# Optimization experiments

Measured on AMD Instinct MI355X. Metric: run time of the kernel, lower is better.

## Reference

```python
import jax, jax.numpy as jnp
import numpy as np


def maxpool2x2(x):
    # NCHW 2x2 max pool, stride 2
    return jax.lax.reduce_window(x, -jnp.inf, jax.lax.max, (1, 1, 2, 2), (1, 1, 2, 2), 'VALID')


def _xavier_uniform(k, shape):
    fan_out, fan_in = shape
    lim = np.sqrt(6.0 / (fan_in + fan_out))
    return jax.random.uniform(k, shape, jnp.float32, -lim, lim)


def setup_inputs() -> dict:
    key = jax.random.key(0)
    ks = jax.random.split(key, 5)
    C = 64
    x = jax.random.normal(ks[0], (4, C, 128, 128), jnp.float32)
    Wq = _xavier_uniform(ks[1], (C // 8, C))  # 1x1 conv == channel matmul
    Wk = _xavier_uniform(ks[2], (C // 8, C))
    Wv = _xavier_uniform(ks[3], (C // 2, C))
    Wo = _xavier_uniform(ks[4], (C, C // 2))
    gamma = jnp.full((1,), 0.1, jnp.float32)  # nonzero so attention branch contributes
    return {"x": x, "Wq": Wq, "Wk": Wk, "Wv": Wv, "Wo": Wo, "gamma": gamma}


def reference(x, Wq, Wk, Wv, Wo, gamma):
    b, c, w, h = x.shape
    # 1x1 convs as channel contractions
    q = jnp.einsum('oc,bchw->bohw', Wq, x).reshape(b, c // 8, w * h)          # [b, c/8, k]
    k_ = maxpool2x2(jnp.einsum('oc,bchw->bohw', Wk, x)).reshape(b, c // 8, -1)  # [b, c/8, f]
    v = maxpool2x2(jnp.einsum('oc,bchw->bohw', Wv, x)).reshape(b, c // 2, -1)   # [b, c/2, f]
    # softmax over full-resolution query positions k (last axis), per pooled position f
    weights = jax.nn.softmax(jnp.einsum('bcf,bck->bfk', k_, q), axis=-1)        # [b, f, k]
    out = jnp.einsum('bcf,bfk->bck', v, weights).reshape(b, c // 2, w, h)       # [b, c/2, w, h]
    out = jnp.einsum('oc,bchw->bohw', Wo, out)                                   # [b, c, w, h]
    return gamma * out + x
```

## Files before the change

### kernel.cpp

```cpp
#include <hip/hip_runtime.h>
#include <cstdint>
#include <cstddef>


#define LOG2E 1.44269504088896340736f
#define FE_A 8388608.0f
#define FE_B 1064993098.0f

typedef __attribute__((ext_vector_type(8)))  __bf16 bf8_t;
typedef __attribute__((ext_vector_type(16))) float  fx16;

__device__ __forceinline__ unsigned short f2bf(float f) {
  unsigned int u = __builtin_bit_cast(unsigned int, f);
  u += 0x7FFFu + ((u >> 16) & 1u);
  return (unsigned short)(u >> 16);
}
__device__ __forceinline__ unsigned int pk2(unsigned short lo, unsigned short hi) {
  return (unsigned int)lo | ((unsigned int)hi << 16);
}
__device__ __forceinline__ int pi16(int s) {
  int m = (s >> 2) & 3;
  return (m == 1 || m == 2) ? (s ^ 12) : s;
}
__device__ __forceinline__ unsigned fe_u(float s) {
  return (unsigned)fmaf(s, FE_A, FE_B);
}
__device__ __forceinline__ float fe_f(float s) {
  return __builtin_bit_cast(float, fe_u(s));
}
__device__ __forceinline__ unsigned fe_pk(float s0, float s1) {
  return __builtin_amdgcn_perm(fe_u(s1), fe_u(s0), 0x07060302);
}

__global__ void __launch_bounds__(512) k_qkv(const float* __restrict__ x,
                                             const float* __restrict__ Wq,
                                             const float* __restrict__ Wk,
                                             const float* __restrict__ Wv,
                                             const float* __restrict__ Wo,
                                             unsigned short* __restrict__ Qp,
                                             unsigned short* __restrict__ KpB,
                                             float* __restrict__ Vp,
                                             unsigned short* __restrict__ Wop) {
  if (blockIdx.x == 256) {
    for (int i = threadIdx.x; i < 2048; i += 512) {
      int c = i & 31;
      Wop[i] = f2bf(Wo[(i & ~31) | (c & 16) | pi16(c & 15)]);
    }
    return;
  }
  __shared__ float wst[64][48];
  __shared__ float xs[16][256];
  int t = threadIdx.x;
  for (int i = t; i < 512; i += 512) {
    wst[i & 63][i >> 6] = Wq[i];
    wst[i & 63][8 + (i >> 6)] = Wk[i];
  }
  for (int i = t; i < 2048; i += 512) wst[i & 63][16 + (i >> 6)] = Wv[i];
  int b = blockIdx.x >> 6, frow = blockIdx.x & 63;
  int wvx = t >> 6, rg = wvx & 3, h = wvx >> 2;
  int lane = t & 63, c2 = lane >> 1, cpos = lane & 1;
  int cell = h * 32 + c2, col = h * 64 + lane;
  const float* xb = x + (size_t)b * (64 * 16384) + frow * 256;
  float acc[12][2];
#pragma unroll
  for (int j = 0; j < 12; ++j) { acc[j][0] = 0.f; acc[j][1] = 0.f; }
  int cl = t >> 5, seg = t & 31;
  for (int cc = 0; cc < 4; ++cc) {
    __syncthreads();
    const float4* src =
        reinterpret_cast<const float4*>(xb + (size_t)(cc * 16 + cl) * 16384 + seg * 8);
    float4* dst = reinterpret_cast<float4*>(&xs[cl][seg * 8]);
    dst[0] = src[0]; dst[1] = src[1];
    __syncthreads();
#pragma unroll
    for (int c16 = 0; c16 < 16; ++c16) {
      int c = cc * 16 + c16;
      float xa = xs[c16][col], xo = xs[c16][128 + col];
      float4 w0 = *reinterpret_cast<const float4*>(&wst[c][12 * rg]);
      float4 w1 = *reinterpret_cast<const float4*>(&wst[c][12 * rg + 4]);
      float4 w2 = *reinterpret_cast<const float4*>(&wst[c][12 * rg + 8]);
      float wj[12] = {w0.x, w0.y, w0.z, w0.w, w1.x, w1.y, w1.z, w1.w,
                      w2.x, w2.y, w2.z, w2.w};
#pragma unroll
      for (int j = 0; j < 12; ++j) {
        acc[j][0] = fmaf(wj[j], xa, acc[j][0]);
        acc[j][1] = fmaf(wj[j], xo, acc[j][1]);
      }
    }
  }
  float pm[12];
#pragma unroll
  for (int j = 0; j < 12; ++j) {
    pm[j] = fmaxf(acc[j][0], acc[j][1]);
    pm[j] = fmaxf(pm[j], __shfl_xor(pm[j], 1));
  }
  size_t idx = (size_t)b * 4096 + frow * 64 + cell;
  uint4 z4; z4.x = z4.y = z4.z = z4.w = 0u;
  if (rg == 0) {
#pragma unroll
    for (int p = 0; p < 2; ++p) {
      int kpos = frow * 256 + p * 128 + col;
      uint4 qa;
      qa.x = pk2(f2bf(acc[0][p]), f2bf(acc[1][p]));
      qa.y = pk2(f2bf(acc[2][p]), f2bf(acc[3][p]));
      qa.z = pk2(f2bf(acc[4][p]), f2bf(acc[5][p]));
      qa.w = pk2(f2bf(acc[6][p]), f2bf(acc[7][p]));
      uint4* qdst = reinterpret_cast<uint4*>(Qp + ((size_t)b * 16384 + kpos) * 16);
      qdst[0] = qa; qdst[1] = z4;
    }
    if (cpos == 0) {
      uint2 kw;
      kw.x = pk2(f2bf(pm[8] * LOG2E), f2bf(pm[9] * LOG2E));
      kw.y = pk2(f2bf(pm[10] * LOG2E), f2bf(pm[11] * LOG2E));
      *reinterpret_cast<uint2*>(KpB + idx * 16) = kw;
    }
  } else if (rg == 1) {
    if (cpos == 0) {
      uint2 kw;
      kw.x = pk2(f2bf(pm[0] * LOG2E), f2bf(pm[1] * LOG2E));
      kw.y = pk2(f2bf(pm[2] * LOG2E), f2bf(pm[3] * LOG2E));
      *reinterpret_cast<uint2*>(KpB + idx * 16 + 4) = kw;
      *reinterpret_cast<uint4*>(KpB + idx * 16 + 8) = z4;
      float* vd = Vp + idx * 32;
      *reinterpret_cast<float4*>(vd) = make_float4(pm[4], pm[5], pm[6], pm[7]);
      *reinterpret_cast<float4*>(vd + 4) = make_float4(pm[8], pm[9], pm[10], pm[11]);
    }
  } else if (cpos == 0) {
    float* vd = Vp + idx * 32 + (rg == 2 ? 8 : 20);
#pragma unroll
    for (int j4 = 0; j4 < 3; ++j4)
      *reinterpret_cast<float4*>(vd + 4 * j4) =
          make_float4(pm[4 * j4], pm[4 * j4 + 1], pm[4 * j4 + 2], pm[4 * j4 + 3]);
  }
}

__global__ void __launch_bounds__(1024) k_lsum(const unsigned short* __restrict__ Qp,
                                               const unsigned short* __restrict__ KpB,
                                               float* __restrict__ Lpart) {
  int b = blockIdx.x >> 8, r = blockIdx.x & 255;
  int fg = r >> 1, kh = r & 1;
  int wv = threadIdx.x >> 6, lane = threadIdx.x & 63;
  int half = lane >> 5, l31 = lane & 31;
  bf8_t A = *reinterpret_cast<const bf8_t*>(
      KpB + ((size_t)(b * 4096 + fg * 32 + l31)) * 16 + half * 8);
  const unsigned short* qbase = Qp + ((size_t)b * 16384) * 16 + half * 8;
  fx16 z;
#pragma unroll
  for (int i = 0; i < 16; ++i) z[i] = 0.f;
  float l[16];
#pragma unroll
  for (int i = 0; i < 16; ++i) l[i] = 0.f;
  int t0 = kh * 256 + wv * 16;
  bf8_t B = *reinterpret_cast<const bf8_t*>(qbase + (size_t)(t0 * 32 + l31) * 16);
  for (int i = 0; i < 16; ++i) {
    int tn = t0 + ((i + 1) & 15);
    bf8_t nB = *reinterpret_cast<const bf8_t*>(qbase + (size_t)(tn * 32 + l31) * 16);
    fx16 s = __builtin_amdgcn_mfma_f32_32x32x16_bf16(A, B, z, 0, 0, 0);
#pragma unroll
    for (int r0 = 0; r0 < 16; ++r0) l[r0] += fe_f(s[r0]);
    B = nB;
  }
#pragma unroll
  for (int r0 = 0; r0 < 16; ++r0)
    for (int d = 1; d < 32; d <<= 1) l[r0] += __shfl_xor(l[r0], d);
  __shared__ float sl[16][32];
  if (l31 == 0) {
#pragma unroll
    for (int r0 = 0; r0 < 16; ++r0) {
      int row = (r0 & 3) + 8 * (r0 >> 2) + 4 * half;
      sl[wv][row] = l[r0];
    }
  }
  __syncthreads();
  if (threadIdx.x < 32) {
    float L = 0.f;
#pragma unroll
    for (int w2 = 0; w2 < 16; ++w2) L += sl[w2][threadIdx.x];
    Lpart[(size_t)kh * 16384 + b * 4096 + fg * 32 + threadIdx.x] = L;
  }
}

__global__ void __launch_bounds__(256) k_pack(const float* __restrict__ Vp,
                                              const float* __restrict__ Lpart,
                                              unsigned short* __restrict__ Vpp) {
  int b = blockIdx.x >> 4, f0 = (blockIdx.x & 15) * 256;
  __shared__ unsigned short T[32][264];
  int t = threadIdx.x;
  size_t li = (size_t)b * 4096 + f0 + t;
  float rl = 1.0f / (Lpart[li] + Lpart[16384 + li]);
  const float* vp = Vp + li * 32;
  int fl = (t & ~15) | pi16(t & 15);
  for (int c = 0; c < 32; ++c) T[c][fl] = f2bf(vp[c] * rl);
  __syncthreads();
  for (int u = t; u < 1024; u += 256) {
    int row = u >> 5, e0 = (u & 31) * 8;
    uint4 val = *reinterpret_cast<const uint4*>(&T[row][e0]);
    *reinterpret_cast<uint4*>(Vpp + ((size_t)b * 32 + row) * 4096 + f0 + e0) = val;
  }
}

__global__ void __launch_bounds__(512) k_attn(const unsigned short* __restrict__ Qp,
                                              const unsigned short* __restrict__ KpB,
                                              const unsigned short* __restrict__ Vpp,
                                              const unsigned short* __restrict__ Wop,
                                              const float* __restrict__ x,
                                              const float* __restrict__ gamma,
                                              float* __restrict__ out) {
  int b = blockIdx.x >> 8, kp = blockIdx.x & 255;
  int wv = threadIdx.x >> 6, lane = threadIdx.x & 63;
  int half = lane >> 5, l31 = lane & 31;
  int kbase = kp * 64;
  const unsigned short* qb = Qp + ((size_t)b * 16384 + kbase + l31) * 16 + half * 8;
  bf8_t Bq0 = *reinterpret_cast<const bf8_t*>(qb);
  bf8_t Bq1 = *reinterpret_cast<const bf8_t*>(qb + 32 * 16);
  fx16 z;
#pragma unroll
  for (int i = 0; i < 16; ++i) z[i] = 0.f;
  fx16 acc0 = z, acc1 = z;
  const unsigned short* kpB = KpB + ((size_t)b * 4096 + l31) * 16 + half * 8;
  const unsigned short* vpB = Vpp + ((size_t)(b * 32 + l31)) * 4096 + half * 8;
  int c0 = wv * 16;
  int f0 = c0 * 32;
  bf8_t Ak  = *reinterpret_cast<const bf8_t*>(kpB + (size_t)f0 * 16);
  bf8_t Av0 = *reinterpret_cast<const bf8_t*>(vpB + f0);
  bf8_t Av1 = *reinterpret_cast<const bf8_t*>(vpB + f0 + 16);
  for (int fc = 0; fc < 16; ++fc) {
    int f1 = (c0 + ((fc + 1) & 15)) * 32;
    bf8_t nAk  = *reinterpret_cast<const bf8_t*>(kpB + (size_t)f1 * 16);
    bf8_t nAv0 = *reinterpret_cast<const bf8_t*>(vpB + f1);
    bf8_t nAv1 = *reinterpret_cast<const bf8_t*>(vpB + f1 + 16);
    fx16 s0 = __builtin_amdgcn_mfma_f32_32x32x16_bf16(Ak, Bq0, z, 0, 0, 0);
    fx16 s1 = __builtin_amdgcn_mfma_f32_32x32x16_bf16(Ak, Bq1, z, 0, 0, 0);
    uint4 u00, u01, u10, u11;
    u00.x = fe_pk(s0[0], s0[1]);   u00.y = fe_pk(s0[2], s0[3]);
    u00.z = fe_pk(s0[4], s0[5]);   u00.w = fe_pk(s0[6], s0[7]);
    u01.x = fe_pk(s0[8], s0[9]);   u01.y = fe_pk(s0[10], s0[11]);
    u01.z = fe_pk(s0[12], s0[13]); u01.w = fe_pk(s0[14], s0[15]);
    u10.x = fe_pk(s1[0], s1[1]);   u10.y = fe_pk(s1[2], s1[3]);
    u10.z = fe_pk(s1[4], s1[5]);   u10.w = fe_pk(s1[6], s1[7]);
    u11.x = fe_pk(s1[8], s1[9]);   u11.y = fe_pk(s1[10], s1[11]);
    u11.z = fe_pk(s1[12], s1[13]); u11.w = fe_pk(s1[14], s1[15]);
    bf8_t P00 = __builtin_bit_cast(bf8_t, u00);
    bf8_t P01 = __builtin_bit_cast(bf8_t, u01);
    bf8_t P10 = __builtin_bit_cast(bf8_t, u10);
    bf8_t P11 = __builtin_bit_cast(bf8_t, u11);
    acc0 = __builtin_amdgcn_mfma_f32_32x32x16_bf16(Av0, P00, acc0, 0, 0, 0);
    acc1 = __builtin_amdgcn_mfma_f32_32x32x16_bf16(Av0, P10, acc1, 0, 0, 0);
    acc0 = __builtin_amdgcn_mfma_f32_32x32x16_bf16(Av1, P01, acc0, 0, 0, 0);
    acc1 = __builtin_amdgcn_mfma_f32_32x32x16_bf16(Av1, P11, acc1, 0, 0, 0);
    Ak = nAk; Av0 = nAv0; Av1 = nAv1;
  }
  __shared__ float sacc[4][2][4][64][4];
  if (wv >= 4) {
    int s = wv - 4;
#pragma unroll
    for (int j4 = 0; j4 < 4; ++j4) {
      *reinterpret_cast<float4*>(&sacc[s][0][j4][lane][0]) =
          make_float4(acc0[4 * j4], acc0[4 * j4 + 1], acc0[4 * j4 + 2], acc0[4 * j4 + 3]);
      *reinterpret_cast<float4*>(&sacc[s][1][j4][lane][0]) =
          make_float4(acc1[4 * j4], acc1[4 * j4 + 1], acc1[4 * j4 + 2], acc1[4 * j4 + 3]);
    }
  }
  __syncthreads();
  if (wv >= 4) return;
  int kt = wv & 1, ot = wv >> 1;
  int k = kbase + kt * 32 + l31;
  const float* xp = x + (size_t)b * 64 * 16384 + k;
  float xv[16];
#pragma unroll
  for (int r0 = 0; r0 < 16; ++r0) {
    int row = (r0 & 3) + 8 * (r0 >> 2) + 4 * half + ot * 32;
    xv[r0] = xp[(size_t)row * 16384];
  }
#pragma unroll
  for (int j4 = 0; j4 < 4; ++j4) {
    float4 p0 = *reinterpret_cast<const float4*>(&sacc[wv][0][j4][lane][0]);
    float4 p1 = *reinterpret_cast<const float4*>(&sacc[wv][1][j4][lane][0]);
    p0.x += acc0[4 * j4]; p0.y += acc0[4 * j4 + 1];
    p0.z += acc0[4 * j4 + 2]; p0.w += acc0[4 * j4 + 3];
    p1.x += acc1[4 * j4]; p1.y += acc1[4 * j4 + 1];
    p1.z += acc1[4 * j4 + 2]; p1.w += acc1[4 * j4 + 3];
    *reinterpret_cast<float4*>(&sacc[wv][0][j4][lane][0]) = p0;
    *reinterpret_cast<float4*>(&sacc[wv][1][j4][lane][0]) = p1;
  }
  __syncthreads();
  fx16 tot;
#pragma unroll
  for (int j4 = 0; j4 < 4; ++j4) {
    float4 a0 = *reinterpret_cast<const float4*>(&sacc[0][kt][j4][lane][0]);
    float4 a1 = *reinterpret_cast<const float4*>(&sacc[1][kt][j4][lane][0]);
    float4 a2 = *reinterpret_cast<const float4*>(&sacc[2][kt][j4][lane][0]);
    float4 a3 = *reinterpret_cast<const float4*>(&sacc[3][kt][j4][lane][0]);
    tot[4 * j4]     = (a0.x + a1.x) + (a2.x + a3.x);
    tot[4 * j4 + 1] = (a0.y + a1.y) + (a2.y + a3.y);
    tot[4 * j4 + 2] = (a0.z + a1.z) + (a2.z + a3.z);
    tot[4 * j4 + 3] = (a0.w + a1.w) + (a2.w + a3.w);
  }
  bf8_t Ob0, Ob1;
#pragma unroll
  for (int j = 0; j < 8; ++j) { Ob0[j] = (__bf16)tot[j]; Ob1[j] = (__bf16)tot[8 + j]; }
  const unsigned short* wb = Wop + (ot * 32 + l31) * 32 + half * 8;
  bf8_t Aw0 = *reinterpret_cast<const bf8_t*>(wb);
  bf8_t Aw1 = *reinterpret_cast<const bf8_t*>(wb + 16);
  fx16 y = __builtin_amdgcn_mfma_f32_32x32x16_bf16(Aw0, Ob0, z, 0, 0, 0);
  y = __builtin_amdgcn_mfma_f32_32x32x16_bf16(Aw1, Ob1, y, 0, 0, 0);
  float g = gamma[0];
  float* op = out + (size_t)b * 64 * 16384 + k;
#pragma unroll
  for (int r0 = 0; r0 < 16; ++r0) {
    int row = (r0 & 3) + 8 * (r0 >> 2) + 4 * half + ot * 32;
    op[(size_t)row * 16384] = fmaf(g, y[r0], xv[r0]);
  }
}

extern "C" void kernel_launch(void* const* d_in, const int* in_sizes, int n_in,
                              void* d_out, int out_size, void* d_ws, size_t ws_size,
                              hipStream_t stream) {
  const float* x     = (const float*)d_in[0];
  const float* Wq    = (const float*)d_in[1];
  const float* Wk    = (const float*)d_in[2];
  const float* Wv    = (const float*)d_in[3];
  const float* Wo    = (const float*)d_in[4];
  const float* gamma = (const float*)d_in[5];
  float* out = (float*)d_out;
  char* ws = (char*)d_ws;
  unsigned short* Qp    = (unsigned short*)(ws + 0);
  unsigned short* KpB   = (unsigned short*)(ws + 2097152);
  float*          Vp    = (float*)(ws + 2621440);
  unsigned short* Vpp   = (unsigned short*)(ws + 4718592);
  float*          Lpart = (float*)(ws + 5767168);
  unsigned short* Wop   = (unsigned short*)(ws + 5898240);

  k_qkv <<<dim3(257),  dim3(512),  0, stream>>>(x, Wq, Wk, Wv, Wo, Qp, KpB, Vp, Wop);
  k_lsum<<<dim3(1024), dim3(1024), 0, stream>>>(Qp, KpB, Lpart);
  k_pack<<<dim3(64),   dim3(256),  0, stream>>>(Vp, Lpart, Vpp);
  k_attn<<<dim3(1024), dim3(512),  0, stream>>>(Qp, KpB, Vpp, Wop, x, gamma, out);
}
```

Before: 154.0 us.

## Use split-bf16 MFMA for QKV projection and retile lsum/attn blocks

The QKV projection moves from scalar FMA to MFMA, using a hi/lo bf16 split (three MFMAs per step) to keep near-fp32 accuracy, with x staged in swizzled LDS. The log-sum kernel now has each wave handle two K tiles over 32 Q tiles, with four partial sums per row instead of two. The attention kernel drops to 256-thread blocks where each wave covers 32 f-chunks, and a final wave computes both output-channel halves, removing one LDS reduction round. The aim is to cut ALU time in the projection and reduce block-level reduction and synchronisation overhead, at the cost of more register pressure and less parallelism per block.

After: 154.4 us. About the same (+0.3%).

```diff
diff --git a/kernel.cpp b/kernel.cpp
--- a/kernel.cpp
+++ b/kernel.cpp
@@ -15,6 +15,10 @@
   u += 0x7FFFu + ((u >> 16) & 1u);
   return (unsigned short)(u >> 16);
 }
+__device__ __forceinline__ float bf2f(unsigned short h) {
+  unsigned int u = ((unsigned int)h) << 16;
+  return __builtin_bit_cast(float, u);
+}
 __device__ __forceinline__ unsigned int pk2(unsigned short lo, unsigned short hi) {
   return (unsigned int)lo | ((unsigned int)hi << 16);
 }
@@ -31,6 +35,8 @@
 __device__ __forceinline__ unsigned fe_pk(float s0, float s1) {
   return __builtin_amdgcn_perm(fe_u(s1), fe_u(s0), 0x07060302);
 }
+
+#define MFMA __builtin_amdgcn_mfma_f32_32x32x16_bf16
 
 __global__ void __launch_bounds__(512) k_qkv(const float* __restrict__ x,
                                              const float* __restrict__ Wq,
@@ -48,135 +54,168 @@
     }
     return;
   }
-  __shared__ float wst[64][48];
-  __shared__ float xs[16][256];
+  __shared__ unsigned int xs[256 * 64];
   int t = threadIdx.x;
-  for (int i = t; i < 512; i += 512) {
-    wst[i & 63][i >> 6] = Wq[i];
-    wst[i & 63][8 + (i >> 6)] = Wk[i];
-  }
-  for (int i = t; i < 2048; i += 512) wst[i & 63][16 + (i >> 6)] = Wv[i];
-  int b = blockIdx.x >> 6, frow = blockIdx.x & 63;
-  int wvx = t >> 6, rg = wvx & 3, h = wvx >> 2;
-  int lane = t & 63, c2 = lane >> 1, cpos = lane & 1;
-  int cell = h * 32 + c2, col = h * 64 + lane;
-  const float* xb = x + (size_t)b * (64 * 16384) + frow * 256;
-  float acc[12][2];
-#pragma unroll
-  for (int j = 0; j < 12; ++j) { acc[j][0] = 0.f; acc[j][1] = 0.f; }
-  int cl = t >> 5, seg = t & 31;
-  for (int cc = 0; cc < 4; ++cc) {
-    __syncthreads();
-    const float4* src =
-        reinterpret_cast<const float4*>(xb + (size_t)(cc * 16 + cl) * 16384 + seg * 8);
-    float4* dst = reinterpret_cast<float4*>(&xs[cl][seg * 8]);
-    dst[0] = src[0]; dst[1] = src[1];
-    __syncthreads();
-#pragma unroll
-    for (int c16 = 0; c16 < 16; ++c16) {
-      int c = cc * 16 + c16;
-      float xa = xs[c16][col], xo = xs[c16][128 + col];
-      float4 w0 = *reinterpret_cast<const float4*>(&wst[c][12 * rg]);
-      float4 w1 = *reinterpret_cast<const float4*>(&wst[c][12 * rg + 4]);
-      float4 w2 = *reinterpret_cast<const float4*>(&wst[c][12 * rg + 8]);
-      float wj[12] = {w0.x, w0.y, w0.z, w0.w, w1.x, w1.y, w1.z, w1.w,
-                      w2.x, w2.y, w2.z, w2.w};
-#pragma unroll
-      for (int j = 0; j < 12; ++j) {
-        acc[j][0] = fmaf(wj[j], xa, acc[j][0]);
-        acc[j][1] = fmaf(wj[j], xo, acc[j][1]);
-      }
-    }
-  }
-  float pm[12];
-#pragma unroll
-  for (int j = 0; j < 12; ++j) {
-    pm[j] = fmaxf(acc[j][0], acc[j][1]);
-    pm[j] = fmaxf(pm[j], __shfl_xor(pm[j], 1));
-  }
-  size_t idx = (size_t)b * 4096 + frow * 64 + cell;
-  uint4 z4; z4.x = z4.y = z4.z = z4.w = 0u;
-  if (rg == 0) {
-#pragma unroll
-    for (int p = 0; p < 2; ++p) {
-      int kpos = frow * 256 + p * 128 + col;
-      uint4 qa;
-      qa.x = pk2(f2bf(acc[0][p]), f2bf(acc[1][p]));
-      qa.y = pk2(f2bf(acc[2][p]), f2bf(acc[3][p]));
-      qa.z = pk2(f2bf(acc[4][p]), f2bf(acc[5][p]));
-      qa.w = pk2(f2bf(acc[6][p]), f2bf(acc[7][p]));
-      uint4* qdst = reinterpret_cast<uint4*>(Qp + ((size_t)b * 16384 + kpos) * 16);
-      qdst[0] = qa; qdst[1] = z4;
-    }
-    if (cpos == 0) {
+  int b = blockIdx.x >> 6, T = blockIdx.x & 63;
+  {
+    int pos = t & 255, cslot = t >> 8;
+    const float* xb = x + (size_t)b * (64 * 16384) + T * 256 + pos;
+    int sw = pos & 15;
+    unsigned int* row = xs + pos * 64;
+#pragma unroll
+    for (int i = 0; i < 16; ++i) {
+      int p = cslot * 16 + i;
+      float g0 = xb[(size_t)(2 * p) * 16384];
+      float g1 = xb[(size_t)(2 * p + 1) * 16384];
+      unsigned short h0 = f2bf(g0), h1 = f2bf(g1);
+      unsigned short l0 = f2bf(g0 - bf2f(h0)), l1 = f2bf(g1 - bf2f(h1));
+      int q = p >> 2, d = p & 3;
+      row[((q + sw) & 15) * 4 + d] = pk2(h0, h1);
+      row[((q + 8 + sw) & 15) * 4 + d] = pk2(l0, l1);
+    }
+  }
+  int wv = t >> 6, lane = t & 63;
+  int cg = wv & 3, Mt = wv >> 2;
+  int m = lane & 31, h = lane >> 5;
+  const float* wrow;
+  float scale = 1.0f;
+  bool zero = false;
+  if (Mt == 0) {
+    if (m < 8) wrow = Wq + m * 64;
+    else if (m < 16) { wrow = Wk + (m - 8) * 64; scale = LOG2E; }
+    else wrow = Wv + (m - 16) * 64;
+  } else {
+    if (m < 16) wrow = Wv + (m + 16) * 64;
+    else { wrow = Wq; zero = true; }
+  }
+  bf8_t Ahi[4], Alo[4];
+#pragma unroll
+  for (int kk = 0; kk < 4; ++kk) {
+    unsigned short hi8[8], lo8[8];
+#pragma unroll
+    for (int j = 0; j < 8; ++j) {
+      float w = zero ? 0.f : wrow[kk * 16 + h * 8 + j] * scale;
+      unsigned short wh = f2bf(w);
+      hi8[j] = wh;
+      lo8[j] = f2bf(w - bf2f(wh));
+    }
+    uint4 uh, ul;
+    uh.x = pk2(hi8[0], hi8[1]); uh.y = pk2(hi8[2], hi8[3]);
+    uh.z = pk2(hi8[4], hi8[5]); uh.w = pk2(hi8[6], hi8[7]);
+    ul.x = pk2(lo8[0], lo8[1]); ul.y = pk2(lo8[2], lo8[3]);
+    ul.z = pk2(lo8[4], lo8[5]); ul.w = pk2(lo8[6], lo8[7]);
+    Ahi[kk] = __builtin_bit_cast(bf8_t, uh);
+    Alo[kk] = __builtin_bit_cast(bf8_t, ul);
+  }
+  __syncthreads();
+  fx16 z;
+#pragma unroll
+  for (int i = 0; i < 16; ++i) z[i] = 0.f;
+  fx16 D0 = z, D1 = z;
+#pragma unroll
+  for (int r = 0; r < 2; ++r) {
+    fx16 acc = z;
+    int pos = cg * 32 + r * 128 + (lane & 31);
+    const unsigned int* row = xs + pos * 64;
+    int sw = pos & 15;
+#pragma unroll
+    for (int kk = 0; kk < 4; ++kk) {
+      int q = 2 * kk + h;
+      bf8_t Bh = *reinterpret_cast<const bf8_t*>(&row[((q + sw) & 15) * 4]);
+      bf8_t Bl = *reinterpret_cast<const bf8_t*>(&row[((q + 8 + sw) & 15) * 4]);
+      acc = MFMA(Ahi[kk], Bh, acc, 0, 0, 0);
+      acc = MFMA(Ahi[kk], Bl, acc, 0, 0, 0);
+      acc = MFMA(Alo[kk], Bh, acc, 0, 0, 0);
+    }
+    if (r == 0) D0 = acc; else D1 = acc;
+  }
+  uint2 z2; z2.x = z2.y = 0u;
+  if (Mt == 0) {
+#pragma unroll
+    for (int r = 0; r < 2; ++r) {
+      const fx16& D = r ? D1 : D0;
+      int gpos = T * 256 + r * 128 + cg * 32 + (lane & 31);
+      unsigned short* qd = Qp + ((size_t)b * 16384 + gpos) * 16;
+      uint2 qa;
+      qa.x = pk2(f2bf(D[0]), f2bf(D[1]));
+      qa.y = pk2(f2bf(D[2]), f2bf(D[3]));
+      *reinterpret_cast<uint2*>(qd + h * 4) = qa;
+      *reinterpret_cast<uint2*>(qd + 8 + h * 4) = z2;
+    }
+  }
+  float pm[16];
+#pragma unroll
+  for (int r0 = 0; r0 < 16; ++r0) {
+    float a = fmaxf(D0[r0], __shfl_xor(D0[r0], 1));
+    float bb = fmaxf(D1[r0], __shfl_xor(D1[r0], 1));
+    pm[r0] = fmaxf(a, bb);
+  }
+  if ((lane & 1) == 0) {
+    size_t idx = (size_t)b * 4096 + T * 64 + cg * 16 + ((lane & 31) >> 1);
+    float* vd = Vp + idx * 32;
+    if (Mt == 0) {
       uint2 kw;
-      kw.x = pk2(f2bf(pm[8] * LOG2E), f2bf(pm[9] * LOG2E));
-      kw.y = pk2(f2bf(pm[10] * LOG2E), f2bf(pm[11] * LOG2E));
-      *reinterpret_cast<uint2*>(KpB + idx * 16) = kw;
-    }
-  } else if (rg == 1) {
-    if (cpos == 0) {
-      uint2 kw;
-      kw.x = pk2(f2bf(pm[0] * LOG2E), f2bf(pm[1] * LOG2E));
-      kw.y = pk2(f2bf(pm[2] * LOG2E), f2bf(pm[3] * LOG2E));
-      *reinterpret_cast<uint2*>(KpB + idx * 16 + 4) = kw;
-      *reinterpret_cast<uint4*>(KpB + idx * 16 + 8) = z4;
-      float* vd = Vp + idx * 32;
-      *reinterpret_cast<float4*>(vd) = make_float4(pm[4], pm[5], pm[6], pm[7]);
-      *reinterpret_cast<float4*>(vd + 4) = make_float4(pm[8], pm[9], pm[10], pm[11]);
-    }
-  } else if (cpos == 0) {
-    float* vd = Vp + idx * 32 + (rg == 2 ? 8 : 20);
-#pragma unroll
-    for (int j4 = 0; j4 < 3; ++j4)
-      *reinterpret_cast<float4*>(vd + 4 * j4) =
-          make_float4(pm[4 * j4], pm[4 * j4 + 1], pm[4 * j4 + 2], pm[4 * j4 + 3]);
-  }
-}
-
-__global__ void __launch_bounds__(1024) k_lsum(const unsigned short* __restrict__ Qp,
-                                               const unsigned short* __restrict__ KpB,
-                                               float* __restrict__ Lpart) {
+      kw.x = pk2(f2bf(pm[4]), f2bf(pm[5]));
+      kw.y = pk2(f2bf(pm[6]), f2bf(pm[7]));
+      *reinterpret_cast<uint2*>(KpB + idx * 16 + h * 4) = kw;
+      *reinterpret_cast<float4*>(vd + h * 4) = make_float4(pm[8], pm[9], pm[10], pm[11]);
+      *reinterpret_cast<float4*>(vd + 8 + h * 4) = make_float4(pm[12], pm[13], pm[14], pm[15]);
+    } else {
+      *reinterpret_cast<uint2*>(KpB + idx * 16 + 8 + h * 4) = z2;
+      *reinterpret_cast<float4*>(vd + 16 + h * 4) = make_float4(pm[0], pm[1], pm[2], pm[3]);
+      *reinterpret_cast<float4*>(vd + 24 + h * 4) = make_float4(pm[4], pm[5], pm[6], pm[7]);
+    }
+  }
+}
+
+__global__ void __launch_bounds__(256, 4) k_lsum(const unsigned short* __restrict__ Qp,
+                                                 const unsigned short* __restrict__ KpB,
+                                                 float* __restrict__ Lpart) {
   int b = blockIdx.x >> 8, r = blockIdx.x & 255;
-  int fg = r >> 1, kh = r & 1;
+  int g = r >> 2, kq = r & 3;
   int wv = threadIdx.x >> 6, lane = threadIdx.x & 63;
   int half = lane >> 5, l31 = lane & 31;
-  bf8_t A = *reinterpret_cast<const bf8_t*>(
-      KpB + ((size_t)(b * 4096 + fg * 32 + l31)) * 16 + half * 8);
+  const unsigned short* kb =
+      KpB + ((size_t)(b * 4096 + g * 64 + l31)) * 16 + half * 8;
+  bf8_t A0 = *reinterpret_cast<const bf8_t*>(kb);
+  bf8_t A1 = *reinterpret_cast<const bf8_t*>(kb + 32 * 16);
   const unsigned short* qbase = Qp + ((size_t)b * 16384) * 16 + half * 8;
   fx16 z;
 #pragma unroll
   for (int i = 0; i < 16; ++i) z[i] = 0.f;
-  float l[16];
-#pragma unroll
-  for (int i = 0; i < 16; ++i) l[i] = 0.f;
-  int t0 = kh * 256 + wv * 16;
+  float l[32];
+#pragma unroll
+  for (int i = 0; i < 32; ++i) l[i] = 0.f;
+  int t0 = kq * 128 + wv * 32;
   bf8_t B = *reinterpret_cast<const bf8_t*>(qbase + (size_t)(t0 * 32 + l31) * 16);
-  for (int i = 0; i < 16; ++i) {
-    int tn = t0 + ((i + 1) & 15);
+  for (int i = 0; i < 32; ++i) {
+    int tn = t0 + ((i + 1) & 31);
     bf8_t nB = *reinterpret_cast<const bf8_t*>(qbase + (size_t)(tn * 32 + l31) * 16);
-    fx16 s = __builtin_amdgcn_mfma_f32_32x32x16_bf16(A, B, z, 0, 0, 0);
-#pragma unroll
-    for (int r0 = 0; r0 < 16; ++r0) l[r0] += fe_f(s[r0]);
+    fx16 s0 = MFMA(A0, B, z, 0, 0, 0);
+    fx16 s1 = MFMA(A1, B, z, 0, 0, 0);
+#pragma unroll
+    for (int r0 = 0; r0 < 16; ++r0) l[r0] += fe_f(s0[r0]);
+#pragma unroll
+    for (int r0 = 0; r0 < 16; ++r0) l[16 + r0] += fe_f(s1[r0]);
     B = nB;
   }
 #pragma unroll
-  for (int r0 = 0; r0 < 16; ++r0)
+  for (int r0 = 0; r0 < 32; ++r0)
     for (int d = 1; d < 32; d <<= 1) l[r0] += __shfl_xor(l[r0], d);
-  __shared__ float sl[16][32];
+  __shared__ float sl[4][2][32];
   if (l31 == 0) {
 #pragma unroll
     for (int r0 = 0; r0 < 16; ++r0) {
       int row = (r0 & 3) + 8 * (r0 >> 2) + 4 * half;
-      sl[wv][row] = l[r0];
+      sl[wv][0][row] = l[r0];
+      sl[wv][1][row] = l[16 + r0];
     }
   }
   __syncthreads();
-  if (threadIdx.x < 32) {
-    float L = 0.f;
-#pragma unroll
-    for (int w2 = 0; w2 < 16; ++w2) L += sl[w2][threadIdx.x];
-    Lpart[(size_t)kh * 16384 + b * 4096 + fg * 32 + threadIdx.x] = L;
+  if (threadIdx.x < 64) {
+    int fgi = threadIdx.x >> 5, row = threadIdx.x & 31;
+    float L = sl[0][fgi][row] + sl[1][fgi][row] + sl[2][fgi][row] + sl[3][fgi][row];
+    Lpart[(size_t)kq * 16384 + b * 4096 + g * 64 + fgi * 32 + row] = L;
   }
 }
 
@@ -184,28 +223,29 @@
                                               const float* __restrict__ Lpart,
                                               unsigned short* __restrict__ Vpp) {
   int b = blockIdx.x >> 4, f0 = (blockIdx.x & 15) * 256;
-  __shared__ unsigned short T[32][264];
+  __shared__ unsigned short Tt[32][264];
   int t = threadIdx.x;
   size_t li = (size_t)b * 4096 + f0 + t;
-  float rl = 1.0f / (Lpart[li] + Lpart[16384 + li]);
+  float L = Lpart[li] + Lpart[li + 16384] + Lpart[li + 32768] + Lpart[li + 49152];
+  float rl = 1.0f / L;
   const float* vp = Vp + li * 32;
   int fl = (t & ~15) | pi16(t & 15);
-  for (int c = 0; c < 32; ++c) T[c][fl] = f2bf(vp[c] * rl);
+  for (int c = 0; c < 32; ++c) Tt[c][fl] = f2bf(vp[c] * rl);
   __syncthreads();
   for (int u = t; u < 1024; u += 256) {
     int row = u >> 5, e0 = (u & 31) * 8;
-    uint4 val = *reinterpret_cast<const uint4*>(&T[row][e0]);
+    uint4 val = *reinterpret_cast<const uint4*>(&Tt[row][e0]);
     *reinterpret_cast<uint4*>(Vpp + ((size_t)b * 32 + row) * 4096 + f0 + e0) = val;
   }
 }
 
-__global__ void __launch_bounds__(512) k_attn(const unsigned short* __restrict__ Qp,
-                                              const unsigned short* __restrict__ KpB,
-                                              const unsigned short* __restrict__ Vpp,
-                                              const unsigned short* __restrict__ Wop,
-                                              const float* __restrict__ x,
-                                              const float* __restrict__ gamma,
-                                              float* __restrict__ out) {
+__global__ void __launch_bounds__(256, 4) k_attn(const unsigned short* __restrict__ Qp,
+                                                 const unsigned short* __restrict__ KpB,
+                                                 const unsigned short* __restrict__ Vpp,
+                                                 const unsigned short* __restrict__ Wop,
+                                                 const float* __restrict__ x,
+                                                 const float* __restrict__ gamma,
+                                                 float* __restrict__ out) {
   int b = blockIdx.x >> 8, kp = blockIdx.x & 255;
   int wv = threadIdx.x >> 6, lane = threadIdx.x & 63;
   int half = lane >> 5, l31 = lane & 31;
@@ -219,18 +259,18 @@
   fx16 acc0 = z, acc1 = z;
   const unsigned short* kpB = KpB + ((size_t)b * 4096 + l31) * 16 + half * 8;
   const unsigned short* vpB = Vpp + ((size_t)(b * 32 + l31)) * 4096 + half * 8;
-  int c0 = wv * 16;
+  int c0 = wv * 32;
   int f0 = c0 * 32;
   bf8_t Ak  = *reinterpret_cast<const bf8_t*>(kpB + (size_t)f0 * 16);
   bf8_t Av0 = *reinterpret_cast<const bf8_t*>(vpB + f0);
   bf8_t Av1 = *reinterpret_cast<const bf8_t*>(vpB + f0 + 16);
-  for (int fc = 0; fc < 16; ++fc) {
-    int f1 = (c0 + ((fc + 1) & 15)) * 32;
+  for (int fc = 0; fc < 32; ++fc) {
+    int f1 = (c0 + ((fc + 1) & 31)) * 32;
     bf8_t nAk  = *reinterpret_cast<const bf8_t*>(kpB + (size_t)f1 * 16);
     bf8_t nAv0 = *reinterpret_cast<const bf8_t*>(vpB + f1);
     bf8_t nAv1 = *reinterpret_cast<const bf8_t*>(vpB + f1 + 16);
-    fx16 s0 = __builtin_amdgcn_mfma_f32_32x32x16_bf16(Ak, Bq0, z, 0, 0, 0);
-    fx16 s1 = __builtin_amdgcn_mfma_f32_32x32x16_bf16(Ak, Bq1, z, 0, 0, 0);
+    fx16 s0 = MFMA(Ak, Bq0, z, 0, 0, 0);
+    fx16 s1 = MFMA(Ak, Bq1, z, 0, 0, 0);
     uint4 u00, u01, u10, u11;
     u00.x = fe_pk(s0[0], s0[1]);   u00.y = fe_pk(s0[2], s0[3]);
     u00.z = fe_pk(s0[4], s0[5]);   u00.w = fe_pk(s0[6], s0[7]);
@@ -244,46 +284,32 @@
     bf8_t P01 = __builtin_bit_cast(bf8_t, u01);
     bf8_t P10 = __builtin_bit_cast(bf8_t, u10);
     bf8_t P11 = __builtin_bit_cast(bf8_t, u11);
-    acc0 = __builtin_amdgcn_mfma_f32_32x32x16_bf16(Av0, P00, acc0, 0, 0, 0);
-    acc1 = __builtin_amdgcn_mfma_f32_32x32x16_bf16(Av0, P10, acc1, 0, 0, 0);
-    acc0 = __builtin_amdgcn_mfma_f32_32x32x16_bf16(Av1, P01, acc0, 0, 0, 0);
-    acc1 = __builtin_amdgcn_mfma_f32_32x32x16_bf16(Av1, P11, acc1, 0, 0, 0);
+    acc0 = MFMA(Av0, P00, acc0, 0, 0, 0);
+    acc1 = MFMA(Av0, P10, acc1, 0, 0, 0);
+    acc0 = MFMA(Av1, P01, acc0, 0, 0, 0);
+    acc1 = MFMA(Av1, P11, acc1, 0, 0, 0);
     Ak = nAk; Av0 = nAv0; Av1 = nAv1;
   }
   __shared__ float sacc[4][2][4][64][4];
-  if (wv >= 4) {
-    int s = wv - 4;
-#pragma unroll
-    for (int j4 = 0; j4 < 4; ++j4) {
-      *reinterpret_cast<float4*>(&sacc[s][0][j4][lane][0]) =
-          make_float4(acc0[4 * j4], acc0[4 * j4 + 1], acc0[4 * j4 + 2], acc0[4 * j4 + 3]);
-      *reinterpret_cast<float4*>(&sacc[s][1][j4][lane][0]) =
-          make_float4(acc1[4 * j4], acc1[4 * j4 + 1], acc1[4 * j4 + 2], acc1[4 * j4 + 3]);
-    }
+#pragma unroll
+  for (int j4 = 0; j4 < 4; ++j4) {
+    *reinterpret_cast<float4*>(&sacc[wv][0][j4][lane][0]) =
+        make_float4(acc0[4 * j4], acc0[4 * j4 + 1], acc0[4 * j4 + 2], acc0[4 * j4 + 3]);
+    *reinterpret_cast<float4*>(&sacc[wv][1][j4][lane][0]) =
+        make_float4(acc1[4 * j4], acc1[4 * j4 + 1], acc1[4 * j4 + 2], acc1[4 * j4 + 3]);
   }
   __syncthreads();
-  if (wv >= 4) return;
-  int kt = wv & 1, ot = wv >> 1;
+  if (wv >= 2) return;
+  int kt = wv;
   int k = kbase + kt * 32 + l31;
   const float* xp = x + (size_t)b * 64 * 16384 + k;
-  float xv[16];
+  float xv0[16], xv1[16];
 #pragma unroll
   for (int r0 = 0; r0 < 16; ++r0) {
-    int row = (r0 & 3) + 8 * (r0 >> 2) + 4 * half + ot * 32;
-    xv[r0] = xp[(size_t)row * 16384];
-  }
-#pragma unroll
-  for (int j4 = 0; j4 < 4; ++j4) {
-    float4 p0 = *reinterpret_cast<const float4*>(&sacc[wv][0][j4][lane][0]);
-    float4 p1 = *reinterpret_cast<const float4*>(&sacc[wv][1][j4][lane][0]);
-    p0.x += acc0[4 * j4]; p0.y += acc0[4 * j4 + 1];
-    p0.z += acc0[4 * j4 + 2]; p0.w += acc0[4 * j4 + 3];
-    p1.x += acc1[4 * j4]; p1.y += acc1[4 * j4 + 1];
-    p1.z += acc1[4 * j4 + 2]; p1.w += acc1[4 * j4 + 3];
-    *reinterpret_cast<float4*>(&sacc[wv][0][j4][lane][0]) = p0;
-    *reinterpret_cast<float4*>(&sacc[wv][1][j4][lane][0]) = p1;
-  }
-  __syncthreads();
+    int row = (r0 & 3) + 8 * (r0 >> 2) + 4 * half;
+    xv0[r0] = xp[(size_t)row * 16384];
+    xv1[r0] = xp[(size_t)(row + 32) * 16384];
+  }
   fx16 tot;
 #pragma unroll
   for (int j4 = 0; j4 < 4; ++j4) {
@@ -299,17 +325,22 @@
   bf8_t Ob0, Ob1;
 #pragma unroll
   for (int j = 0; j < 8; ++j) { Ob0[j] = (__bf16)tot[j]; Ob1[j] = (__bf16)tot[8 + j]; }
-  const unsigned short* wb = Wop + (ot * 32 + l31) * 32 + half * 8;
-  bf8_t Aw0 = *reinterpret_cast<const bf8_t*>(wb);
-  bf8_t Aw1 = *reinterpret_cast<const bf8_t*>(wb + 16);
-  fx16 y = __builtin_amdgcn_mfma_f32_32x32x16_bf16(Aw0, Ob0, z, 0, 0, 0);
-  y = __builtin_amdgcn_mfma_f32_32x32x16_bf16(Aw1, Ob1, y, 0, 0, 0);
+  const unsigned short* wb = Wop + l31 * 32 + half * 8;
+  bf8_t Aw00 = *reinterpret_cast<const bf8_t*>(wb);
+  bf8_t Aw01 = *reinterpret_cast<const bf8_t*>(wb + 16);
+  bf8_t Aw10 = *reinterpret_cast<const bf8_t*>(wb + 1024);
+  bf8_t Aw11 = *reinterpret_cast<const bf8_t*>(wb + 1024 + 16);
+  fx16 y0 = MFMA(Aw00, Ob0, z, 0, 0, 0);
+  y0 = MFMA(Aw01, Ob1, y0, 0, 0, 0);
+  fx16 y1 = MFMA(Aw10, Ob0, z, 0, 0, 0);
+  y1 = MFMA(Aw11, Ob1, y1, 0, 0, 0);
   float g = gamma[0];
   float* op = out + (size_t)b * 64 * 16384 + k;
 #pragma unroll
   for (int r0 = 0; r0 < 16; ++r0) {
-    int row = (r0 & 3) + 8 * (r0 >> 2) + 4 * half + ot * 32;
-    op[(size_t)row * 16384] = fmaf(g, y[r0], xv[r0]);
+    int row = (r0 & 3) + 8 * (r0 >> 2) + 4 * half;
+    op[(size_t)row * 16384]        = fmaf(g, y0[r0], xv0[r0]);
+    op[(size_t)(row + 32) * 16384] = fmaf(g, y1[r0], xv1[r0]);
   }
 }
 
@@ -329,10 +360,10 @@
   float*          Vp    = (float*)(ws + 2621440);
   unsigned short* Vpp   = (unsigned short*)(ws + 4718592);
   float*          Lpart = (float*)(ws + 5767168);
-  unsigned short* Wop   = (unsigned short*)(ws + 5898240);
-
-  k_qkv <<<dim3(257),  dim3(512),  0, stream>>>(x, Wq, Wk, Wv, Wo, Qp, KpB, Vp, Wop);
-  k_lsum<<<dim3(1024), dim3(1024), 0, stream>>>(Qp, KpB, Lpart);
-  k_pack<<<dim3(64),   dim3(256),  0, stream>>>(Vp, Lpart, Vpp);
-  k_attn<<<dim3(1024), dim3(512),  0, stream>>>(Qp, KpB, Vpp, Wop, x, gamma, out);
-}
+  unsigned short* Wop   = (unsigned short*)(ws + 6029312);
+
+  k_qkv <<<dim3(257),  dim3(512), 0, stream>>>(x, Wq, Wk, Wv, Wo, Qp, KpB, Vp, Wop);
+  k_lsum<<<dim3(1024), dim3(256), 0, stream>>>(Qp, KpB, Lpart);
+  k_pack<<<dim3(64),   dim3(256), 0, stream>>>(Vp, Lpart, Vpp);
+  k_attn<<<dim3(1024), dim3(256), 0, stream>>>(Qp, KpB, Vpp, Wop, x, gamma, out);
+}
```
